# Optimization experiments

Hardware: AMD Instinct MI355X
Metric: run time of the kernel (lower is better)

## Reference

```python
import jax, jax.numpy as jnp
import numpy as np

SINGLE_DIM = 256
PAIR_DIM = 64
MAX_REL_POS = 32
LN_EPS = 1e-5


def setup_inputs() -> dict:
    key = jax.random.key(0)
    ks = jax.random.split(key, 6)
    B, N = 2, 1024
    single_repr = jax.random.normal(ks[0], (B, N, SINGLE_DIM), dtype=jnp.float32)
    # Linear(single_dim*2 -> pair_dim)
    lim = 1.0 / np.sqrt(2 * SINGLE_DIM)
    W = jax.random.uniform(ks[1], (2 * SINGLE_DIM, PAIR_DIM), minval=-lim, maxval=lim, dtype=jnp.float32)
    b = jax.random.uniform(ks[2], (PAIR_DIM,), minval=-lim, maxval=lim, dtype=jnp.float32)
    # LayerNorm(pair_dim)
    gamma = jnp.ones((PAIR_DIM,), dtype=jnp.float32)
    beta = jnp.zeros((PAIR_DIM,), dtype=jnp.float32)
    # Embedding(2*max_rel_pos+1, pair_dim)
    embed = jax.random.normal(ks[3], (2 * MAX_REL_POS + 1, PAIR_DIM), dtype=jnp.float32)
    return {"single_repr": single_repr, "W": W, "b": b, "gamma": gamma, "beta": beta, "embed": embed}


def reference(single_repr, W, b, gamma, beta, embed):
    B, N, d = single_repr.shape
    # Split the Linear weight: cat([s_i, s_j]) @ W == s_i @ W_i + s_j @ W_j.
    # This avoids materializing the [B,N,N,2d] concat tensor (outer-sum trick).
    W_i, W_j = W[:d], W[d:]                       # [d, pair_dim] each
    proj_i = jnp.einsum('bnd,dp->bnp', single_repr, W_i)  # [B,N,P]
    proj_j = jnp.einsum('bnd,dp->bnp', single_repr, W_j)  # [B,N,P]
    x = proj_i[:, :, None, :] + proj_j[:, None, :, :] + b  # [B,N,N,P]
    # LayerNorm over last dim
    mu = jnp.mean(x, axis=-1, keepdims=True)
    var = jnp.mean((x - mu) ** 2, axis=-1, keepdims=True)
    x = (x - mu) * jax.lax.rsqrt(var + LN_EPS) * gamma + beta
    x = jax.nn.relu(x)
    # Relative position embedding
    pos = jnp.arange(N)
    rel = jnp.clip(pos[None, :] - pos[:, None], -MAX_REL_POS, MAX_REL_POS) + MAX_REL_POS  # [N,N]
    x = x + embed[rel][None]  # broadcast over batch
    return x
```

## Files before the change

kernel.cpp:

```cpp
#include <hip/hip_runtime.h>

#define SINGLE_DIM 256
#define PAIR_DIM   64
#define MAX_REL    32
#define LN_EPS     1e-5f
#define N_FIXED    1024

typedef float vfloat4 __attribute__((ext_vector_type(4)));

__global__ __launch_bounds__(256) void proj_kernel(
    const float* __restrict__ s,
    const float* __restrict__ W,
    const float* __restrict__ bias,
    float* __restrict__ proj)
{
    __shared__ float lds[2][SINGLE_DIM];
    const int row0 = blockIdx.x * 2;
    const int t = threadIdx.x;

    ((float2*)(&lds[0][0]))[t] = ((const float2*)(s + (size_t)row0 * SINGLE_DIM))[t];
    __syncthreads();

    const int row  = t >> 7;
    const int c    = t & 127;
    const int half = c >> 6;
    const int p    = c & 63;

    const float* wcol = W + half * (SINGLE_DIM * PAIR_DIM) + p;
    const float* srow = lds[row];

    float acc = (half == 0) ? bias[p] : 0.f;
    #pragma unroll 8
    for (int d = 0; d < SINGLE_DIM; ++d)
        acc += srow[d] * wcol[d * PAIR_DIM];

    proj[(size_t)(row0 + row) * 128 + c] = acc;
}

__global__ __launch_bounds__(256) void pair_kernel(
    const float* __restrict__ proj,
    const float* __restrict__ gamma,
    const float* __restrict__ beta,
    const float* __restrict__ embed,
    float* __restrict__ out)
{
    const int t  = threadIdx.x;
    const int g  = t >> 4;
    const int p0 = (t & 15) * 4;
    const int bid = blockIdx.x;
    const int bi    = bid >> 4;
    const int jbase = (bid & 15) * 64 + g;
    const int i = bi & (N_FIXED - 1);
    const int b = bi >> 10;

    const float4 pi4 = *(const float4*)(proj + (size_t)bi * 128 + p0);
    const float4 g4  = *(const float4*)(gamma + p0);
    const float4 b4  = *(const float4*)(beta + p0);

    float4 v[4];
    float  s[4], ss[4];
    #pragma unroll
    for (int k = 0; k < 4; ++k) {
        const int j = jbase + 16 * k;
        const float4 pj4 = *(const float4*)(proj + (size_t)(b * N_FIXED + j) * 128 + 64 + p0);
        v[k].x = pi4.x + pj4.x;
        v[k].y = pi4.y + pj4.y;
        v[k].z = pi4.z + pj4.z;
        v[k].w = pi4.w + pj4.w;
        s[k]  = v[k].x + v[k].y + v[k].z + v[k].w;
        ss[k] = v[k].x * v[k].x + v[k].y * v[k].y + v[k].z * v[k].z + v[k].w * v[k].w;
    }

    #pragma unroll
    for (int mask = 1; mask < 16; mask <<= 1) {
        #pragma unroll
        for (int k = 0; k < 4; ++k) {
            s[k]  += __shfl_xor(s[k],  mask, 64);
            ss[k] += __shfl_xor(ss[k], mask, 64);
        }
    }

    #pragma unroll
    for (int k = 0; k < 4; ++k) {
        const int j = jbase + 16 * k;
        const float mean = s[k] * (1.f / PAIR_DIM);
        const float var  = ss[k] * (1.f / PAIR_DIM) - mean * mean;
        const float rstd = rsqrtf(var + LN_EPS);

        int rel = j - i;
        rel = (rel < -MAX_REL) ? -MAX_REL : (rel > MAX_REL ? MAX_REL : rel);
        rel += MAX_REL;
        const float4 e4 = *(const float4*)(embed + rel * PAIR_DIM + p0);

        vfloat4 o;
        o.x = fmaxf((v[k].x - mean) * rstd * g4.x + b4.x, 0.f) + e4.x;
        o.y = fmaxf((v[k].y - mean) * rstd * g4.y + b4.y, 0.f) + e4.y;
        o.z = fmaxf((v[k].z - mean) * rstd * g4.z + b4.z, 0.f) + e4.z;
        o.w = fmaxf((v[k].w - mean) * rstd * g4.w + b4.w, 0.f) + e4.w;

        __builtin_nontemporal_store(o,
            (vfloat4*)(out + ((size_t)bi * N_FIXED + j) * PAIR_DIM + p0));
    }
}

extern "C" void kernel_launch(void* const* d_in, const int* in_sizes, int n_in,
                              void* d_out, int out_size, void* d_ws, size_t ws_size,
                              hipStream_t stream) {
    const float* s     = (const float*)d_in[0];
    const float* W     = (const float*)d_in[1];
    const float* bias  = (const float*)d_in[2];
    const float* gamma = (const float*)d_in[3];
    const float* beta  = (const float*)d_in[4];
    const float* embed = (const float*)d_in[5];
    float* out  = (float*)d_out;
    float* proj = (float*)d_ws;

    const int BN = in_sizes[0] / SINGLE_DIM;

    proj_kernel<<<BN / 2, 256, 0, stream>>>(s, W, bias, proj);

    const int blocks = BN * (N_FIXED / 64);
    pair_kernel<<<blocks, 256, 0, stream>>>(proj, gamma, beta, embed, out);
}
```

Baseline: 538.6 us.

## Precompute LayerNorm mean/rstd via per-row stats and pairwise dot-product GEMM

Adds per-row sum and sum-of-squares output to the projection kernel, plus a new tiled GEMM kernel that computes the i·j cross term. Together these give the LayerNorm mean and rstd for every (i,j) pair, stored in a float2 matrix. The pair kernel then reads these precomputed stats instead of doing cross-lane shuffle reductions. The cost is an extra launch plus writing and reading a B*N*N float2 buffer (16 MB), and the E[x^2]-mean^2 form may lose precision. It falls back to the old path if the workspace is too small.

```diff
diff --git a/kernel.cpp b/kernel.cpp
--- a/kernel.cpp
+++ b/kernel.cpp
@@ -5,6 +5,7 @@
 #define MAX_REL    32
 #define LN_EPS     1e-5f
 #define N_FIXED    1024
+#define ST_STRIDE  68
 
 typedef float vfloat4 __attribute__((ext_vector_type(4)));
 
@@ -12,7 +13,8 @@
     const float* __restrict__ s,
     const float* __restrict__ W,
     const float* __restrict__ bias,
-    float* __restrict__ proj)
+    float* __restrict__ proj,
+    float* __restrict__ rowstats)
 {
     __shared__ float lds[2][SINGLE_DIM];
     const int row0 = blockIdx.x * 2;
@@ -35,6 +37,135 @@
         acc += srow[d] * wcol[d * PAIR_DIM];
 
     proj[(size_t)(row0 + row) * 128 + c] = acc;
+
+    if (rowstats) {
+        float sv = acc, qv = acc * acc;
+        #pragma unroll
+        for (int mask = 1; mask < 64; mask <<= 1) {
+            sv += __shfl_xor(sv, mask, 64);
+            qv += __shfl_xor(qv, mask, 64);
+        }
+        if ((t & 63) == 0)
+            *(float2*)(rowstats + (size_t)(row0 + row) * 4 + half * 2) =
+                make_float2(sv, qv);
+    }
+}
+
+__global__ __launch_bounds__(256) void stats_kernel(
+    const float* __restrict__ proj,
+    const float* __restrict__ rowstats,
+    float2* __restrict__ M)
+{
+    __shared__ __align__(16) float A [64 * ST_STRIDE];
+    __shared__ __align__(16) float Bt[64 * ST_STRIDE];
+
+    const int t   = threadIdx.x;
+    const int bid = blockIdx.x;
+    const int b   = bid >> 8;
+    const int it  = (bid >> 4) & 15;
+    const int jt  = bid & 15;
+    const int i0  = b * N_FIXED + it * 64;
+    const int j0  = b * N_FIXED + jt * 64;
+
+    #pragma unroll
+    for (int x = 0; x < 4; ++x) {
+        const int idx = t + 256 * x;
+        const int r   = idx >> 4;
+        const int c4  = idx & 15;
+        float4 va = *(const float4*)(proj + (size_t)(i0 + r) * 128 + c4 * 4);
+        float4 vb = *(const float4*)(proj + (size_t)(j0 + r) * 128 + 64 + c4 * 4);
+        *(float4*)(A  + r * ST_STRIDE + c4 * 4) = va;
+        *(float4*)(Bt + r * ST_STRIDE + c4 * 4) = vb;
+    }
+    __syncthreads();
+
+    const int tx = t & 15, ty = t >> 4;
+    float acc[4][4] = {};
+    #pragma unroll
+    for (int kk = 0; kk < 16; ++kk) {
+        float4 a[4], bb[4];
+        #pragma unroll
+        for (int r = 0; r < 4; ++r)
+            a[r] = *(const float4*)(A + (ty * 4 + r) * ST_STRIDE + kk * 4);
+        #pragma unroll
+        for (int c = 0; c < 4; ++c)
+            bb[c] = *(const float4*)(Bt + (tx + 16 * c) * ST_STRIDE + kk * 4);
+        #pragma unroll
+        for (int r = 0; r < 4; ++r)
+            #pragma unroll
+            for (int c = 0; c < 4; ++c)
+                acc[r][c] += a[r].x * bb[c].x + a[r].y * bb[c].y
+                           + a[r].z * bb[c].z + a[r].w * bb[c].w;
+    }
+
+    float2 si[4], sj[4];
+    #pragma unroll
+    for (int r = 0; r < 4; ++r)
+        si[r] = *(const float2*)(rowstats + (size_t)(i0 + ty * 4 + r) * 4);
+    #pragma unroll
+    for (int c = 0; c < 4; ++c)
+        sj[c] = *(const float2*)(rowstats + (size_t)(j0 + tx + 16 * c) * 4 + 2);
+
+    #pragma unroll
+    for (int r = 0; r < 4; ++r) {
+        const size_t mrow = (size_t)(i0 + ty * 4 + r) * N_FIXED;
+        #pragma unroll
+        for (int c = 0; c < 4; ++c) {
+            const float mean = (si[r].x + sj[c].x) * (1.f / PAIR_DIM);
+            const float ex2  = (si[r].y + sj[c].y + 2.f * acc[r][c]) * (1.f / PAIR_DIM);
+            const float rstd = rsqrtf(ex2 - mean * mean + LN_EPS);
+            M[mrow + jt * 64 + tx + 16 * c] = make_float2(mean, rstd);
+        }
+    }
+}
+
+__global__ __launch_bounds__(256) void pair_fast_kernel(
+    const float* __restrict__ proj,
+    const float2* __restrict__ M,
+    const float* __restrict__ gamma,
+    const float* __restrict__ beta,
+    const float* __restrict__ embed,
+    float* __restrict__ out)
+{
+    const int t  = threadIdx.x;
+    const int g  = t >> 4;
+    const int p0 = (t & 15) * 4;
+    const int bid = blockIdx.x;
+    const int bi    = bid >> 4;
+    const int jbase = (bid & 15) * 64 + g;
+    const int i = bi & (N_FIXED - 1);
+
+    const float4 pi4 = *(const float4*)(proj + (size_t)bi * 128 + p0);
+    const float4 g4  = *(const float4*)(gamma + p0);
+    const float4 b4  = *(const float4*)(beta + p0);
+    const size_t mrow = (size_t)bi * N_FIXED;
+
+    #pragma unroll
+    for (int k = 0; k < 4; ++k) {
+        const int j = jbase + 16 * k;
+        const float4 pj4 = *(const float4*)(proj + mrow * 0 + (size_t)((bi >> 10) * N_FIXED + j) * 128 + 64 + p0);
+        const float2 mr  = M[mrow + j];
+        const float mean = mr.x, rstd = mr.y;
+
+        const float Gx = g4.x * rstd, Gy = g4.y * rstd,
+                    Gz = g4.z * rstd, Gw = g4.w * rstd;
+        const float Bx = fmaf(-mean, Gx, b4.x), By = fmaf(-mean, Gy, b4.y),
+                    Bz = fmaf(-mean, Gz, b4.z), Bw = fmaf(-mean, Gw, b4.w);
+
+        int rel = j - i;
+        rel = (rel < -MAX_REL) ? -MAX_REL : (rel > MAX_REL ? MAX_REL : rel);
+        rel += MAX_REL;
+        const float4 e4 = *(const float4*)(embed + rel * PAIR_DIM + p0);
+
+        vfloat4 o;
+        o.x = fmaxf(fmaf(pi4.x + pj4.x, Gx, Bx), 0.f) + e4.x;
+        o.y = fmaxf(fmaf(pi4.y + pj4.y, Gy, By), 0.f) + e4.y;
+        o.z = fmaxf(fmaf(pi4.z + pj4.z, Gz, Bz), 0.f) + e4.z;
+        o.w = fmaxf(fmaf(pi4.w + pj4.w, Gw, Bw), 0.f) + e4.w;
+
+        __builtin_nontemporal_store(o,
+            (vfloat4*)(out + ((size_t)bi * N_FIXED + j) * PAIR_DIM + p0));
+    }
 }
 
 __global__ __launch_bounds__(256) void pair_kernel(
@@ -113,12 +244,30 @@
     const float* beta  = (const float*)d_in[4];
     const float* embed = (const float*)d_in[5];
     float* out  = (float*)d_out;
-    float* proj = (float*)d_ws;
 
     const int BN = in_sizes[0] / SINGLE_DIM;
-
-    proj_kernel<<<BN / 2, 256, 0, stream>>>(s, W, bias, proj);
-
-    const int blocks = BN * (N_FIXED / 64);
-    pair_kernel<<<blocks, 256, 0, stream>>>(proj, gamma, beta, embed, out);
-}
+    const int B  = BN / N_FIXED;
+
+    const size_t off_proj = 0;
+    const size_t sz_proj  = (size_t)BN * 128 * sizeof(float);
+    const size_t off_rs   = off_proj + sz_proj;
+    const size_t sz_rs    = (size_t)BN * 4 * sizeof(float);
+    const size_t off_M    = off_rs + sz_rs;
+    const size_t sz_M     = (size_t)BN * N_FIXED * sizeof(float2);
+    const size_t need     = off_M + sz_M;
+
+    float*  proj     = (float*)((char*)d_ws + off_proj);
+    float*  rowstats = (float*)((char*)d_ws + off_rs);
+    float2* M        = (float2*)((char*)d_ws + off_M);
+
+    const int pair_blocks = BN * (N_FIXED / 64);
+
+    if (ws_size >= need) {
+        proj_kernel<<<BN / 2, 256, 0, stream>>>(s, W, bias, proj, rowstats);
+        stats_kernel<<<B * 16 * 16, 256, 0, stream>>>(proj, rowstats, M);
+        pair_fast_kernel<<<pair_blocks, 256, 0, stream>>>(proj, M, gamma, beta, embed, out);
+    } else {
+        proj_kernel<<<BN / 2, 256, 0, stream>>>(s, W, bias, proj, nullptr);
+        pair_kernel<<<pair_blocks, 256, 0, stream>>>(proj, gamma, beta, embed, out);
+    }
+}
```

Result: no change. 539.0 us (+0.1%).

## Precompute per-row LayerNorm stats and reduce pair kernel to one DPP dot reduction

Applied to the files above, without the earlier changes.

The projection kernel now also writes per-row sum and sum-of-squares for the i and j halves. The pair kernel gets each pair's mean and variance from these stats plus a single cross dot product, reduced over 16 lanes with DPP row operations instead of 8 xor shuffles. The normalization is folded into one fma per element, and launch bounds add an occupancy hint. The kernel is bound by its output writes, so the saved ALU and shuffle work may not show up, and the E[x^2]-mean^2 form is less numerically stable.

```diff
diff --git a/kernel.cpp b/kernel.cpp
--- a/kernel.cpp
+++ b/kernel.cpp
@@ -8,11 +8,24 @@
 
 typedef float vfloat4 __attribute__((ext_vector_type(4)));
 
+#define DPP_ADD(x, ctrl)                                                    \
+    ((x) + __int_as_float(__builtin_amdgcn_update_dpp(                      \
+               0, __float_as_int(x), (ctrl), 0xf, 0xf, true)))
+
+__device__ __forceinline__ float rowsum16(float x) {
+    x = DPP_ADD(x, 0x128);
+    x = DPP_ADD(x, 0x124);
+    x = DPP_ADD(x, 0x122);
+    x = DPP_ADD(x, 0x121);
+    return x;
+}
+
 __global__ __launch_bounds__(256) void proj_kernel(
     const float* __restrict__ s,
     const float* __restrict__ W,
     const float* __restrict__ bias,
-    float* __restrict__ proj)
+    float* __restrict__ proj,
+    float* __restrict__ rowstats)
 {
     __shared__ float lds[2][SINGLE_DIM];
     const int row0 = blockIdx.x * 2;
@@ -35,6 +48,81 @@
         acc += srow[d] * wcol[d * PAIR_DIM];
 
     proj[(size_t)(row0 + row) * 128 + c] = acc;
+
+    if (rowstats) {
+        float sv = acc, qv = acc * acc;
+        #pragma unroll
+        for (int mask = 1; mask < 64; mask <<= 1) {
+            sv += __shfl_xor(sv, mask, 64);
+            qv += __shfl_xor(qv, mask, 64);
+        }
+        if ((t & 63) == 0)
+            *(float2*)(rowstats + (size_t)(row0 + row) * 4 + half * 2) =
+                make_float2(sv, qv);
+    }
+}
+
+__global__ __launch_bounds__(256, 6) void pair_v3_kernel(
+    const float* __restrict__ proj,
+    const float* __restrict__ rowstats,
+    const float* __restrict__ gamma,
+    const float* __restrict__ beta,
+    const float* __restrict__ embed,
+    float* __restrict__ out)
+{
+    const int t  = threadIdx.x;
+    const int g  = t >> 4;
+    const int p0 = (t & 15) * 4;
+    const int bid = blockIdx.x;
+    const int bi    = bid >> 4;
+    const int jbase = (bid & 15) * 64 + g;
+    const int i = bi & (N_FIXED - 1);
+    const int b = bi >> 10;
+
+    const float4 pi4 = *(const float4*)(proj + (size_t)bi * 128 + p0);
+    const float4 g4  = *(const float4*)(gamma + p0);
+    const float4 b4  = *(const float4*)(beta + p0);
+    const float2 rsi = *(const float2*)(rowstats + (size_t)bi * 4);
+
+    #pragma unroll
+    for (int k = 0; k < 4; ++k) {
+        const int j = jbase + 16 * k;
+        const size_t jrow = (size_t)b * N_FIXED + j;
+        const float4 pj4 = *(const float4*)(proj + jrow * 128 + 64 + p0);
+        const float2 rsj = *(const float2*)(rowstats + jrow * 4 + 2);
+
+        float4 v;
+        v.x = pi4.x + pj4.x;
+        v.y = pi4.y + pj4.y;
+        v.z = pi4.z + pj4.z;
+        v.w = pi4.w + pj4.w;
+
+        float dot = pi4.x * pj4.x + pi4.y * pj4.y + pi4.z * pj4.z + pi4.w * pj4.w;
+        dot = rowsum16(dot);
+
+        const float mean = (rsi.x + rsj.x) * (1.f / PAIR_DIM);
+        const float ex2  = (rsi.y + rsj.y + 2.f * dot) * (1.f / PAIR_DIM);
+        const float rstd = rsqrtf(ex2 - mean * mean + LN_EPS);
+
+        const float Gx = g4.x * rstd, Gy = g4.y * rstd,
+                    Gz = g4.z * rstd, Gw = g4.w * rstd;
+        const float Bx = fmaf(-mean, Gx, b4.x), By = fmaf(-mean, Gy, b4.y),
+                    Bz = fmaf(-mean, Gz, b4.z), Bw = fmaf(-mean, Gw, b4.w);
+
+        int rel = j - i;
+        rel = (rel < -MAX_REL) ? -MAX_REL : (rel > MAX_REL ? MAX_REL : rel);
+        rel += MAX_REL;
+        const float4 e4 = *(const float4*)(embed + rel * PAIR_DIM + p0);
+
+        vfloat4 o;
+        o.x = fmaxf(fmaf(v.x, Gx, Bx), 0.f) + e4.x;
+        o.y = fmaxf(fmaf(v.y, Gy, By), 0.f) + e4.y;
+        o.z = fmaxf(fmaf(v.z, Gz, Bz), 0.f) + e4.z;
+        o.w = fmaxf(fmaf(v.w, Gw, Bw), 0.f) + e4.w;
+
+        __builtin_nontemporal_store(o,
+            (vfloat4*)(out + ((size_t)bi * N_FIXED + j) * PAIR_DIM + p0));
+    }
 }
 
 __global__ __launch_bounds__(256) void pair_kernel(
@@ -113,12 +201,22 @@
     const float* beta  = (const float*)d_in[4];
     const float* embed = (const float*)d_in[5];
     float* out  = (float*)d_out;
-    float* proj = (float*)d_ws;
 
     const int BN = in_sizes[0] / SINGLE_DIM;
 
-    proj_kernel<<<BN / 2, 256, 0, stream>>>(s, W, bias, proj);
-
-    const int blocks = BN * (N_FIXED / 64);
-    pair_kernel<<<blocks, 256, 0, stream>>>(proj, gamma, beta, embed, out);
-}
+    const size_t sz_proj = (size_t)BN * 128 * sizeof(float);
+    const size_t sz_rs   = (size_t)BN * 4 * sizeof(float);
+    float* proj     = (float*)d_ws;
+    float* rowstats = (float*)((char*)d_ws + sz_proj);
+
+    const int pair_blocks = BN * (N_FIXED / 64);
+
+    if (ws_size >= sz_proj + sz_rs) {
+        proj_kernel<<<BN / 2, 256, 0, stream>>>(s, W, bias, proj, rowstats);
+        pair_v3_kernel<<<pair_blocks, 256, 0, stream>>>(proj, rowstats, gamma,
+                                                        beta, embed, out);
+    } else {
+        proj_kernel<<<BN / 2, 256, 0, stream>>>(s, W, bias, proj, nullptr);
+        pair_kernel<<<pair_blocks, 256, 0, stream>>>(proj, gamma, beta, embed, out);
+    }
+}
```

After: 529.8 us. About the same (-1.6%).
